# Performance work log

Measured on AMD Instinct MI355X. Metric: run time of the kernel, lower is better.

The kernel has to match this reference:

```python
import jax, jax.numpy as jnp
import numpy as np

B, T, D = 2, 2048, 2048
H, DH = 32, 64
GN_EPS = DH * 1e-5  # GroupNorm eps = head_dim * norm_eps


def _lora(x, A, Bm, bias, act):
    h = x @ A.T
    if act == 'tanh':
        h = jnp.tanh(h)
    elif act == 'sigmoid':
        h = jax.nn.sigmoid(h)
    y = h @ Bm.T
    if bias is not None:
        y = y + bias
    return y


def setup_inputs() -> dict:
    key = jax.random.key(0)
    ks = jax.random.split(key, 24)
    def nrm(i, shape, s):
        return jax.random.normal(ks[i], shape, jnp.float32) * s
    return {
        'hidden_states': nrm(0, (B, T, D), 1.0),
        'v_state': nrm(1, (B, T, D), 1.0),
        'x_x': nrm(2, (6, D), 0.3),
        'k_k': 0.85 + nrm(3, (D,), 0.05),
        'k_a': 1.0 + nrm(4, (D,), 0.05),
        'r_k': nrm(5, (H, DH), 0.1),
        'Wr': nrm(6, (D, D), 0.02),
        'Wk': nrm(7, (D, D), 0.02),
        'Wv': nrm(8, (D, D), 0.02),
        'Wo': nrm(9, (D, D), 0.02),
        'wA': nrm(10, (64, D), 0.02), 'wB': nrm(11, (D, 64), 0.02), 'wb': nrm(12, (D,), 0.5),
        'vA': nrm(13, (16, D), 0.02), 'vB': nrm(14, (D, 16), 0.02), 'vb': jnp.zeros((D,), jnp.float32),
        'aA': nrm(15, (64, D), 0.02), 'aB': nrm(16, (D, 64), 0.02), 'ab': jnp.zeros((D,), jnp.float32),
        'gA': nrm(17, (128, D), 0.02), 'gB': nrm(18, (D, 128), 0.02),
        'gn_w': jnp.ones((D,), jnp.float32), 'gn_b': jnp.zeros((D,), jnp.float32),
    }


def reference(hidden_states, v_state, x_x, k_k, k_a, r_k, Wr, Wk, Wv, Wo,
              wA, wB, wb, vA, vB, vb, aA, aB, ab, gA, gB, gn_w, gn_b):
    b, t, d = hidden_states.shape
    # time_shift: shifted[t] = x[t-1], shifted[0] = 0
    shifted = jnp.pad(hidden_states, ((0, 0), (1, 0), (0, 0)))[:, :t]
    delta = shifted - hidden_states
    xm = hidden_states[None] + delta[None] * x_x[:, None, None, :]  # [6,B,T,D]
    xr, xw, xk, xv, xa, xg = xm[0], xm[1], xm[2], xm[3], xm[4], xm[5]

    r = xr @ Wr.T
    w = -jax.nn.softplus(-_lora(xw, wA, wB, wb, 'tanh')) - 0.5  # log decay, < -0.5
    k = xk @ Wk.T
    v = xv @ Wv.T
    # layer_idx != 0: v = lerp(v, v_state, sigmoid(v_lora(xv)))
    v = v + jax.nn.sigmoid(_lora(xv, vA, vB, vb, None)) * (v_state - v)
    a = jax.nn.sigmoid(_lora(xa, aA, aB, ab, None))
    g = _lora(xg, gA, gB, None, 'sigmoid')

    kk = (k * k_k).reshape(b, t, H, DH)
    kk = kk / jnp.maximum(jnp.linalg.norm(kk, axis=-1, keepdims=True), 1e-12)
    k = k * (1.0 + (a - 1.0) * k_a)

    r_h = r.reshape(b, t, H, DH)
    w_h = w.reshape(b, t, H, DH)
    k_h = k.reshape(b, t, H, DH)
    v_h = v.reshape(b, t, H, DH)
    a_h = a.reshape(b, t, H, DH)
    tm = lambda x: jnp.swapaxes(x, 0, 1)  # [B,T,H,DH] -> [T,B,H,DH]

    # RWKV7 DPLR delta rule: S = diag(exp(w)) S; S += b (a^T S) + k v^T; o = r^T S
    def step(S, xs):
        q_t, w_t, k_t, v_t, at, bt = xs  # each [B,H,DH]
        S = S * jnp.exp(w_t)[..., None]
        sa = jnp.einsum('bhk,bhkv->bhv', at, S)
        S = S + bt[..., None] * sa[..., None, :] + k_t[..., None] * v_t[..., None, :]
        return S, jnp.einsum('bhk,bhkv->bhv', q_t, S)

    S0 = jnp.zeros((b, H, DH, DH), hidden_states.dtype)
    _, o = jax.lax.scan(step, S0,
                        (tm(r_h), tm(w_h), tm(k_h), tm(v_h), tm(-kk), tm(kk * a_h)))
    o = jnp.swapaxes(o, 0, 1)  # [B,T,H,DH]

    # GroupNorm over each head's channels
    mu = o.mean(-1, keepdims=True)
    var = jnp.mean((o - mu) ** 2, axis=-1, keepdims=True)
    on = ((o - mu) / jnp.sqrt(var + GN_EPS)).reshape(b, t, d) * gn_w + gn_b

    on = on + ((r_h * k_h * r_k).sum(-1, keepdims=True) * v_h).reshape(b, t, d)
    return (on * g) @ Wo.T
```

## Files before the change

kernel.cpp:

```cpp
#include <hip/hip_runtime.h>
#include <hip/hip_bf16.h>
#include <math.h>


typedef __attribute__((ext_vector_type(8))) unsigned short ushort8;
typedef __attribute__((ext_vector_type(8))) _Float16 f16x8;
typedef __attribute__((ext_vector_type(4))) float f32x4;
typedef __attribute__((ext_vector_type(2))) float f32x2;

__device__ inline unsigned short f2h(float f) {
    _Float16 h = (_Float16)f;
    return __builtin_bit_cast(unsigned short, h);
}
__device__ inline float h2f(unsigned short u) {
    return (float)__builtin_bit_cast(_Float16, u);
}
__device__ inline float sigm(float x) { return 1.f / (1.f + expf(-x)); }

template <int CTRL>
__device__ __forceinline__ float rrot(float x) {
    int xi = __builtin_bit_cast(int, x);
    int yi = __builtin_amdgcn_update_dpp(xi, xi, CTRL, 0xf, 0xf, true);
    return x + __builtin_bit_cast(float, yi);
}
// ... 19 lines not shown
    x = rrot<0x128>(x);
    return red32(red16(x));
}

__device__ __forceinline__ void gld16(void* lds, const void* g)
{
    __builtin_amdgcn_global_load_lds(
        (const __attribute__((address_space(1))) void*)g,
        (__attribute__((address_space(3))) void*)lds, 16, 0, 0);
}
__device__ __forceinline__ void gld4(void* lds, const void* g)
{
    __builtin_amdgcn_global_load_lds(
        (const __attribute__((address_space(1))) void*)g,
        (__attribute__((address_space(3))) void*)lds, 4, 0, 0);
}

__global__ void mixcvt6_h(const float* __restrict__ in, const float* __restrict__ x_x,
                          unsigned short* __restrict__ oR, unsigned short* __restrict__ oK,
                          unsigned short* __restrict__ ow, unsigned short* __restrict__ oa,
                          unsigned short* __restrict__ og, unsigned short* __restrict__ ov,
                          int T, int D, int total8)
{
    int i = blockIdx.x * 256 + threadIdx.x;
    if (i >= total8) return;
    const size_t e = (size_t)i * 8;
    float a[8];
    *(float4*)&a[0] = *(const float4*)(in + e);
    *(float4*)&a[4] = *(const float4*)(in + e + 4);
    const int m = (int)(e / D);
// ... 17 lines not shown
        rr[j] = f2h(a[j] + dl * xxr[j]);
        rk[j] = f2h(a[j] + dl * xxk[j]);
        rw[j] = f2h(a[j] + dl * xxw[j]);
        ra[j] = f2h(a[j] + dl * xxa[j]);
        rg[j] = f2h(a[j] + dl * xxg[j]);
        rv[j] = f2h(a[j] + dl * xxv[j]);
    }
    *(ushort8*)(oR + e) = rr;
    *(ushort8*)(oK + e) = rk;
    *(ushort8*)(ow + e) = rw;
    *(ushort8*)(oa + e) = ra;
    *(ushort8*)(og + e) = rg;
    *(ushort8*)(ov + e) = rv;
}

__global__ void wcvt2_h(const float* __restrict__ in0, const float* __restrict__ in1,
                        unsigned short* __restrict__ hi0, unsigned short* __restrict__ hi1,
                        int total8)
{
    int i = blockIdx.x * 256 + threadIdx.x;
    if (i >= total8) return;
    const float* in = (blockIdx.y == 0) ? in0 : in1;
    unsigned short* hi = (blockIdx.y == 0) ? hi0 : hi1;
    const size_t e = (size_t)i * 8;
    float a[8];
    *(float4*)&a[0] = *(const float4*)(in + e);
    *(float4*)&a[4] = *(const float4*)(in + e + 4);
    ushort8 h8;
    #pragma unroll
    for (int j = 0; j < 8; ++j) h8[j] = f2h(a[j]);
    *(ushort8*)(hi + e) = h8;
}

__global__ void wcvt_all(const float* __restrict__ Wr, const float* __restrict__ Wk,
                         const float* __restrict__ Wv, const float* __restrict__ wB,
                         const float* __restrict__ aB, const float* __restrict__ gB,
                         unsigned short* __restrict__ oWr, unsigned short* __restrict__ oWk,
                         unsigned short* __restrict__ oWv, unsigned short* __restrict__ owB,
                         unsigned short* __restrict__ oaB, unsigned short* __restrict__ ogB,
                         int nBig, int nSm, int nG)
{
    const int y = blockIdx.y;
    const float* in;
    unsigned short* hi;
    int lim;
    if (y == 0)      { in = Wr; hi = oWr; lim = nBig; }
    else if (y == 1) { in = Wk; hi = oWk; lim = nBig; }
    else if (y == 2) { in = Wv; hi = oWv; lim = nBig; }
    else if (y == 3) { in = wB; hi = owB; lim = nSm; }
    else if (y == 4) { in = aB; hi = oaB; lim = nSm; }
    else             { in = gB; hi = ogB; lim = nG; }
    int i = blockIdx.x * 256 + threadIdx.x;
    if (i >= lim) return;
    const size_t e = (size_t)i * 8;
    float a[8];
    *(float4*)&a[0] = *(const float4*)(in + e);
    *(float4*)&a[4] = *(const float4*)(in + e + 4);
    ushort8 h8;
    #pragma unroll
    for (int j = 0; j < 8; ++j) h8[j] = f2h(a[j]);
    *(ushort8*)(hi + e) = h8;
}

__global__ void wcvt_lora(const float* __restrict__ wA, const float* __restrict__ vA,
                          const float* __restrict__ aA, const float* __restrict__ gA,
                          unsigned short* __restrict__ WL, int K)
{
    const int z = blockIdx.y;
    int i = blockIdx.x * 256 + threadIdx.x;
    const size_t e = (size_t)i * 8;
    const int row = (int)(e / K);
    const int col = (int)(e % K);
    const int nv = (z == 0) ? 64 : (z == 1) ? 16 : (z == 2) ? 64 : 128;
    const float* src = (z == 0) ? wA : (z == 1) ? vA : (z == 2) ? aA : gA;
    ushort8 h8;
    if (row < nv) {
        float a[8];
        *(float4*)&a[0] = *(const float4*)(src + (size_t)row * K + col);
        *(float4*)&a[4] = *(const float4*)(src + (size_t)row * K + col + 4);
        #pragma unroll
        for (int j = 0; j < 8; ++j) h8[j] = f2h(a[j]);
    } else {
        #pragma unroll
        for (int j = 0; j < 8; ++j) h8[j] = 0;
    }
    *(ushort8*)(WL + (size_t)z * 128 * K + e) = h8;
}

#define GBM 128
#define GBN 128

template <int TERMS>
__global__ __launch_bounds__(256) void gemm_h2(
    const unsigned short* __restrict__ Ag,
    const unsigned short* __restrict__ Bhg, const unsigned short* __restrict__ Blg,
    float* __restrict__ C, int M, int N, int K, int mode,
    const float* __restrict__ HVp, const float* __restrict__ vBp,
    const float* __restrict__ bias, const float* __restrict__ aux,
    size_t sA, size_t sB, size_t sC)
{
    __shared__ unsigned short As[GBM * 32];
    __shared__ unsigned short Bhs[GBN * 32], Bls[GBN * 32];
    const int z = blockIdx.z;
    Ag  += (size_t)z * sA;
    Bhg += (size_t)z * sB;
    Blg += (size_t)z * sB;
    C   += (size_t)z * sC;
    const int tid = threadIdx.x;
    const int m0 = blockIdx.x * GBM;
    const int n0 = blockIdx.y * GBN;
    const int wave = tid >> 6, lane = tid & 63;
    const int wr = (wave >> 1) * 64, wc = (wave & 1) * 64;
    const int fr = lane & 15, fq = lane >> 4;

    f32x4 acc[4][4];
    #pragma unroll
    for (int i = 0; i < 4; ++i)
        #pragma unroll
        for (int j = 0; j < 4; ++j)
            acc[i][j] = (f32x4){0.f, 0.f, 0.f, 0.f};

    const unsigned short* gsrc;
    unsigned short* lbuf;
    int rofs, nld;
    if (wave == 0)      { gsrc = Ag;  lbuf = As;           rofs = m0;      nld = 4; }
    else if (wave == 1) { gsrc = Ag;  lbuf = As + 64 * 32; rofs = m0 + 64; nld = 4; }
    else if (wave == 2) { gsrc = Bhg; lbuf = Bhs;          rofs = n0;      nld = 8; }
    else                { gsrc = Blg; lbuf = Bls;          rofs = n0;      nld = (TERMS == 2) ? 8 : 0; }
    const unsigned short* gbase = gsrc + (size_t)(rofs + (lane >> 2)) * K + ((lane & 3) << 3);

    for (int k0 = 0; k0 < K; k0 += 32) {
        #pragma unroll
        for (int j = 0; j < 8; ++j)
            if (j < nld)
                gld16(lbuf + j * 16 * 32, gbase + (size_t)(j * 16) * K + k0);
        __syncthreads();

        f16x8 fa[4], fbh[4], fbl[4];
        #pragma unroll
        for (int m = 0; m < 4; ++m)
            fa[m] = *(const f16x8*)&As[(wr + m * 16 + fr) * 32 + fq * 8];
        #pragma unroll
        for (int n = 0; n < 4; ++n) {
            fbh[n] = *(const f16x8*)&Bhs[(wc + n * 16 + fr) * 32 + fq * 8];
            if constexpr (TERMS == 2)
                fbl[n] = *(const f16x8*)&Bls[(wc + n * 16 + fr) * 32 + fq * 8];
        }
        #pragma unroll
        for (int m = 0; m < 4; ++m)
            #pragma unroll
            for (int n = 0; n < 4; ++n) {
                acc[m][n] = __builtin_amdgcn_mfma_f32_16x16x32_f16(fa[m], fbh[n], acc[m][n], 0, 0, 0);
                if constexpr (TERMS == 2)
                    acc[m][n] = __builtin_amdgcn_mfma_f32_16x16x32_f16(fa[m], fbl[n], acc[m][n], 0, 0, 0);
            }
        __syncthreads();
    }

    #pragma unroll
    for (int m = 0; m < 4; ++m) {
        const int row = m0 + wr + m * 16 + fq * 4;
        #pragma unroll
        for (int n = 0; n < 4; ++n) {
            const int col = n0 + wc + n * 16 + fr;
            #pragma unroll
            for (int j = 0; j < 4; ++j) {
                const size_t idx = (size_t)(row + j) * N + col;
                float v = acc[m][n][j];
                if (mode == 4) {
                    const float* hv = HVp + (size_t)(row + j) * 16;
                    const float* vv = vBp + (size_t)col * 16;
                    float yv = 0.f;
                    #pragma unroll
                    for (int kk = 0; kk < 16; ++kk) yv = fmaf(hv[kk], vv[kk], yv);
                    const float sg = sigm(yv + bias[col]);
                    v = v + sg * (aux[idx] - v);
                } else if (mode == 3 && z == 0) {
                    v = 0.6065306597126334f * sigm(v + bias[col]);
                }
                C[idx] = v;
            }
        }
    }
}

__global__ __launch_bounds__(256) void gemm_rkv(
    const unsigned short* __restrict__ Xrk,
    const unsigned short* __restrict__ Xv,
    const unsigned short* __restrict__ Wr16, const unsigned short* __restrict__ Wk16,
    const unsigned short* __restrict__ Wv16,
    float* __restrict__ Cr, float* __restrict__ Ck, float* __restrict__ Cv,
    const float* __restrict__ HVp, const float* __restrict__ vBp,
    const float* __restrict__ vb, const float* __restrict__ vst,
    int M, int N, int K)
{
    __shared__ unsigned short As[GBM * 32];
    __shared__ unsigned short Bhs[GBN * 32];
    const int z = blockIdx.z;
    const unsigned short* Ag = (z == 0) ? Xrk : (z == 1) ? (Xrk + (size_t)M * K) : Xv;
    const unsigned short* Bg = (z == 0) ? Wr16 : (z == 1) ? Wk16 : Wv16;
    float* C = (z == 0) ? Cr : (z == 1) ? Ck : Cv;
    const int tid = threadIdx.x;
    const int m0 = blockIdx.x * GBM;
    const int n0 = blockIdx.y * GBN;
    const int wave = tid >> 6, lane = tid & 63;
    const int wr = (wave >> 1) * 64, wc = (wave & 1) * 64;
    const int fr = lane & 15, fq = lane >> 4;

    f32x4 acc[4][4];
    #pragma unroll
    for (int i = 0; i < 4; ++i)
        #pragma unroll
        for (int j = 0; j < 4; ++j)
            acc[i][j] = (f32x4){0.f, 0.f, 0.f, 0.f};

    const unsigned short* gsrc;
    unsigned short* lbuf;
    int rofs, nld;
    if (wave == 0)      { gsrc = Ag; lbuf = As;           rofs = m0;      nld = 4; }
    else if (wave == 1) { gsrc = Ag; lbuf = As + 64 * 32; rofs = m0 + 64; nld = 4; }
    else if (wave == 2) { gsrc = Bg; lbuf = Bhs;          rofs = n0;      nld = 8; }
    else                { gsrc = Bg; lbuf = Bhs;          rofs = n0;      nld = 0; }
    const unsigned short* gbase = gsrc + (size_t)(rofs + (lane >> 2)) * K + ((lane & 3) << 3);

    for (int k0 = 0; k0 < K; k0 += 32) {
        #pragma unroll
        for (int j = 0; j < 8; ++j)
            if (j < nld)
                gld16(lbuf + j * 16 * 32, gbase + (size_t)(j * 16) * K + k0);
        __syncthreads();

        f16x8 fa[4], fb[4];
        #pragma unroll
        for (int m = 0; m < 4; ++m)
            fa[m] = *(const f16x8*)&As[(wr + m * 16 + fr) * 32 + fq * 8];
        #pragma unroll
        for (int n = 0; n < 4; ++n)
            fb[n] = *(const f16x8*)&Bhs[(wc + n * 16 + fr) * 32 + fq * 8];
        #pragma unroll
        for (int m = 0; m < 4; ++m)
            #pragma unroll
            for (int n = 0; n < 4; ++n)
                acc[m][n] = __builtin_amdgcn_mfma_f32_16x16x32_f16(fa[m], fb[n], acc[m][n], 0, 0, 0);
        __syncthreads();
    }

    #pragma unroll
    for (int m = 0; m < 4; ++m) {
        const int row = m0 + wr + m * 16 + fq * 4;
        #pragma unroll
        for (int n = 0; n < 4; ++n) {
            const int col = n0 + wc + n * 16 + fr;
            #pragma unroll
            for (int j = 0; j < 4; ++j) {
                const size_t idx = (size_t)(row + j) * N + col;
                float v = acc[m][n][j];
                if (z == 2) {
                    const float* hv = HVp + (size_t)(row + j) * 16;
                    const float* vv = vBp + (size_t)col * 16;
                    float yv = 0.f;
                    #pragma unroll
                    for (int kk = 0; kk < 16; ++kk) yv = fmaf(hv[kk], vv[kk], yv);
                    const float sg = sigm(yv + vb[col]);
                    v = v + sg * (vst[idx] - v);
                }
                C[idx] = v;
            }
        }
    }
}

__global__ __launch_bounds__(256) void lora1_h(
    const unsigned short* __restrict__ Xbase,
    const unsigned short* __restrict__ WL,
    unsigned short* __restrict__ HW16, float* __restrict__ HV,
    unsigned short* __restrict__ HA16, unsigned short* __restrict__ HG16,
    int M, int K, size_t NE)
{
    __shared__ unsigned short As[GBM * 32];
    __shared__ unsigned short Bhs[GBN * 32];
    const int z = blockIdx.z;
    const size_t zofs = (z == 0) ? 0 : (z == 1) ? 3 * NE : (z == 2) ? NE : 2 * NE;
    const unsigned short* Ag = Xbase + zofs;
    const unsigned short* Bg = WL + (size_t)z * 128 * K;
    const int tid = threadIdx.x;
    const int m0 = blockIdx.x * GBM;
    const int wave = tid >> 6, lane = tid & 63;
    const int wr = (wave >> 1) * 64, wc = (wave & 1) * 64;
    const int fr = lane & 15, fq = lane >> 4;

    f32x4 acc[4][4];
    #pragma unroll
    for (int i = 0; i < 4; ++i)
        #pragma unroll
        for (int j = 0; j < 4; ++j)
            acc[i][j] = (f32x4){0.f, 0.f, 0.f, 0.f};

    const unsigned short* gsrc;
    unsigned short* lbuf;
    int rofs, nld;
    if (wave == 0)      { gsrc = Ag; lbuf = As;           rofs = m0;      nld = 4; }
    else if (wave == 1) { gsrc = Ag; lbuf = As + 64 * 32; rofs = m0 + 64; nld = 4; }
    else if (wave == 2) { gsrc = Bg; lbuf = Bhs;          rofs = 0;       nld = 8; }
    else                { gsrc = Bg; lbuf = Bhs;          rofs = 0;       nld = 0; }
    const unsigned short* gbase = gsrc + (size_t)(rofs + (lane >> 2)) * K + ((lane & 3) << 3);

    for (int k0 = 0; k0 < K; k0 += 32) {
        #pragma unroll
        for (int j = 0; j < 8; ++j)
            if (j < nld)
                gld16(lbuf + j * 16 * 32, gbase + (size_t)(j * 16) * K + k0);
        __syncthreads();

        f16x8 fa[4], fb[4];
        #pragma unroll
        for (int m = 0; m < 4; ++m)
            fa[m] = *(const f16x8*)&As[(wr + m * 16 + fr) * 32 + fq * 8];
        #pragma unroll
        for (int n = 0; n < 4; ++n)
            fb[n] = *(const f16x8*)&Bhs[(wc + n * 16 + fr) * 32 + fq * 8];
        #pragma unroll
        for (int m = 0; m < 4; ++m)
            #pragma unroll
            for (int n = 0; n < 4; ++n)
                acc[m][n] = __builtin_amdgcn_mfma_f32_16x16x32_f16(fa[m], fb[n], acc[m][n], 0, 0, 0);
        __syncthreads();
    }

    #pragma unroll
    for (int m = 0; m < 4; ++m) {
        const int row = m0 + wr + m * 16 + fq * 4;
        #pragma unroll
        for (int n = 0; n < 4; ++n) {
            const int col = wc + n * 16 + fr;
            #pragma unroll
            for (int j = 0; j < 4; ++j) {
                const float v = acc[m][n][j];
                const int r = row + j;
                if (z == 0)      { if (col < 64) HW16[(size_t)r * 64 + col] = f2h(tanhf(v)); }
                else if (z == 1) { if (col < 16) HV[(size_t)r * 16 + col] = v; }
                else if (z == 2) { if (col < 64) HA16[(size_t)r * 64 + col] = f2h(v); }
                else             { HG16[(size_t)r * 128 + col] = f2h(sigm(v)); }
// ... 169 lines not shown

    if (bid < 512) {
        if (tid >= 64) return;
        scan_core(smemf, bid, tid, EW, R, Kf, Vf, KK, BV, O, T, H);
        return;
    }
    if (bid < 1024) {
        unsigned short* As  = (unsigned short*)smemf;
        unsigned short* Bhs = As + GBM * 32;
        const int bid2 = bid - 512;
        const int m0 = (bid2 >> 4) * GBM;
        const int n0 = (bid2 & 15) * GBN;
        const int wave = tid >> 6, lane = tid & 63;
        const int wr = (wave >> 1) * 64, wc = (wave & 1) * 64;
        const int fr = lane & 15, fq = lane >> 4;
        const int K = 128;

        f32x4 acc[4][4];
        #pragma unroll
        for (int i = 0; i < 4; ++i)
            #pragma unroll
            for (int j = 0; j < 4; ++j)
                acc[i][j] = (f32x4){0.f, 0.f, 0.f, 0.f};

        const unsigned short* gsrc;
        unsigned short* lbuf;
        int rofs, nld;
        if (wave == 0)      { gsrc = HG16; lbuf = As;           rofs = m0;      nld = 4; }
        else if (wave == 1) { gsrc = HG16; lbuf = As + 64 * 32; rofs = m0 + 64; nld = 4; }
        else if (wave == 2) { gsrc = gb16; lbuf = Bhs;          rofs = n0;      nld = 8; }
        else                { gsrc = gb16; lbuf = Bhs;          rofs = n0;      nld = 0; }
        const unsigned short* gbase = gsrc + (size_t)(rofs + (lane >> 2)) * K + ((lane & 3) << 3);

        for (int k0 = 0; k0 < K; k0 += 32) {
            #pragma unroll
            for (int j = 0; j < 8; ++j)
                if (j < nld)
                    gld16(lbuf + j * 16 * 32, gbase + (size_t)(j * 16) * K + k0);
            __syncthreads();
            f16x8 fa[4], fb[4];
            #pragma unroll
            for (int m = 0; m < 4; ++m)
                fa[m] = *(const f16x8*)&As[(wr + m * 16 + fr) * 32 + fq * 8];
            #pragma unroll
            for (int n = 0; n < 4; ++n)
                fb[n] = *(const f16x8*)&Bhs[(wc + n * 16 + fr) * 32 + fq * 8];
            #pragma unroll
            for (int m = 0; m < 4; ++m)
                #pragma unroll
                for (int n = 0; n < 4; ++n)
                    acc[m][n] = __builtin_amdgcn_mfma_f32_16x16x32_f16(fa[m], fb[n], acc[m][n], 0, 0, 0);
            __syncthreads();
        }
        #pragma unroll
        for (int m = 0; m < 4; ++m) {
            const int row = m0 + wr + m * 16 + fq * 4;
            #pragma unroll
            for (int n = 0; n < 4; ++n) {
                const int col = n0 + wc + n * 16 + fr;
                #pragma unroll
                for (int j = 0; j < 4; ++j)
                    G16[(size_t)(row + j) * D + col] = f2h(acc[m][n][j]);
            }
        }
        return;
    }
    {
        int i = (bid - 1024) * 256 + tid;
// ... 88 lines not shown
    unsigned short* HA16 = HW16 + (size_t)M * 64;
    unsigned short* HG16 = HA16 + (size_t)M * 64;
    float* HV = (float*)(HG16 + (size_t)M * 128);
    float* W6 = SMALL + (size_t)M * 272;

    dim3 blk(256);
    const int nMix = (int)(NE / 8);
    const int nW   = (int)(DD / 8);
    const int nSm  = (int)(D * 64 / 8);
    const int nG   = (int)(D * 128 / 8);
    const float* nf = nullptr;

    unsigned short* X2   = (unsigned short*)W1;
    unsigned short* X4   = (unsigned short*)W4;
    unsigned short* WRK  = (unsigned short*)W3;
    unsigned short* WL   = (unsigned short*)W0;

    hipLaunchKernelGGL(mixcvt6_h, dim3(nMix / 256), blk, 0, stream,
                       hid, x_x, X2, X2 + NE, X4, X4 + NE, X4 + 2 * NE, X4 + 3 * NE, T, D, nMix);

    hipLaunchKernelGGL(wcvt_lora, dim3(128, 4), blk, 0, stream, wA, vA, aA, gA, WL, D);

    if (fused) {
        unsigned short* W6s  = (unsigned short*)W6;
        unsigned short* G16p = W6s;
        unsigned short* WvWo = W6s + NE;
        unsigned short* gb16 = W6s + NE + DD;
        unsigned short* wB16 = gb16 + (size_t)D * 128;
        unsigned short* aB16 = wB16 + (size_t)D * 64;

        hipLaunchKernelGGL(wcvt_all, dim3(nW / 256, 6), blk, 0, stream,
                           Wr, Wk, Wv, wB, aB, gB,
                           WRK, WRK + DD, WvWo, wB16, aB16, gb16, nW, nSm, nG);

        hipLaunchKernelGGL(lora1_h, dim3(M / GBM, 1, 4), blk, 0, stream,
                           X4, WL, HW16, HV, HA16, HG16, M, D, NE);

        hipLaunchKernelGGL(gemm_rkv, dim3(M / GBM, D / GBN, 3), blk, 0, stream,
                           X2, X4 + 3 * NE, WRK, WRK + DD, WvWo,
                           W0, W2, W3, HV, vB, vb, vst, M, D, D);

        hipLaunchKernelGGL((gemm_h2<1>), dim3(M / GBM, D / GBN, 2), blk, 0, stream,
                           HW16, wB16, wB16, W1, M, D, 64, 3, nf, nf, wb, nf,
                           (size_t)M * 64, (size_t)D * 64, 4 * NE);

        const int totalW = M * H;
        hipLaunchKernelGGL(ka_epi, dim3(totalW / 4), blk, 0, stream, W2, W5, W4, k_k, k_a, ab, totalW, H);

        hipLaunchKernelGGL(scan_fused, dim3(512 + 512 + 2048), blk, 0, stream,
                           W1, W0, W2, W3, W4, W5, out,
                           HG16, gb16, G16p, Wo, WvWo, nW, T, H, M, D);

        unsigned short* ON16 = (unsigned short*)W1;
        hipLaunchKernelGGL(gn_bonus, dim3(totalW / 4), blk, 0, stream, out, W0, W2, W3, nf, G16p, r_k, gnw, gnb, ON16, totalW, H, 64.f * 1e-5f);

        hipLaunchKernelGGL((gemm_h2<1>), dim3(M / GBM, D / GBN, 1), blk, 0, stream,
                           ON16, WvWo, WvWo, out, M, D, D, 0, nf, nf, nf, nf, 0, 0, 0);
    } else {
        hipLaunchKernelGGL(wcvt2_h, dim3(nW / 256, 2), blk, 0, stream, Wr, Wk, WRK, WRK + DD, nW);
        hipLaunchKernelGGL(lora1_h, dim3(M / GBM, 1, 4), blk, 0, stream,
                           X4, WL, HW16, HV, HA16, HG16, M, D, NE);
        hipLaunchKernelGGL((gemm_h2<1>), dim3(M / GBM, D / GBN, 2), blk, 0, stream,
                           X2, WRK, WRK, W0, M, D, D, 0, nf, nf, nf, nf,
                           NE, DD, 2 * NE);
        unsigned short* WvH = (unsigned short*)W4;
        hipLaunchKernelGGL(wcvt2_h, dim3(nW / 256, 1), blk, 0, stream, Wv, Wv, WvH, WvH, nW);
        hipLaunchKernelGGL((gemm_h2<1>), dim3(M / GBM, D / GBN, 1), blk, 0, stream,
                           X4 + 3 * NE, WvH, WvH, W3, M, D, D, 4, HV, vB, vb, vst, 0, 0, 0);
        unsigned short* wB16 = (unsigned short*)W4;
        unsigned short* aB16 = wB16 + (size_t)D * 64;
        hipLaunchKernelGGL(wcvt2_h, dim3(nSm / 256, 2), blk, 0, stream, wB, aB, wB16, aB16, nSm);
        hipLaunchKernelGGL((gemm_h2<1>), dim3(M / GBM, D / GBN, 2), blk, 0, stream,
                           HW16, wB16, wB16, W1, M, D, 64, 3, nf, nf, wb, nf,
                           (size_t)M * 64, (size_t)D * 64, 4 * NE);
        const int totalW = M * H;
        hipLaunchKernelGGL(ka_epi, dim3(totalW / 4), blk, 0, stream, W2, W5, W4, k_k, k_a, ab, totalW, H);
// ... 14 lines not shown
```

Measured before the change: 829.7 us.

## Merge prep conversions and independent GEMM launches into fewer mega-kernels

```diff
diff --git a/kernel.cpp b/kernel.cpp
--- a/kernel.cpp
+++ b/kernel.cpp
@@ -57,6 +57,416 @@
     __builtin_amdgcn_global_load_lds(
         (const __attribute__((address_space(1))) void*)g,
         (__attribute__((address_space(3))) void*)lds, 4, 0, 0);
+}
+
+__device__ __forceinline__ void gemm128_loop(
+    const unsigned short* __restrict__ Ag, const unsigned short* __restrict__ Bg,
+    unsigned short* As, unsigned short* Bhs,
+    int m0, int n0, int K, int tid, f32x4 (&acc)[4][4])
+{
+    const int wave = tid >> 6, lane = tid & 63;
+    const int wr = (wave >> 1) * 64, wc = (wave & 1) * 64;
+    const int fr = lane & 15, fq = lane >> 4;
+
+    const unsigned short* gsrc;
+    unsigned short* lbuf;
+    int rofs, nld;
+    if (wave == 0)      { gsrc = Ag; lbuf = As;           rofs = m0;      nld = 4; }
+    else if (wave == 1) { gsrc = Ag; lbuf = As + 64 * 32; rofs = m0 + 64; nld = 4; }
+    else if (wave == 2) { gsrc = Bg; lbuf = Bhs;          rofs = n0;      nld = 8; }
+    else                { gsrc = Bg; lbuf = Bhs;          rofs = n0;      nld = 0; }
+    const unsigned short* gbase = gsrc + (size_t)(rofs + (lane >> 2)) * K + ((lane & 3) << 3);
+
+    for (int k0 = 0; k0 < K; k0 += 32) {
+        #pragma unroll
+        for (int j = 0; j < 8; ++j)
+            if (j < nld)
+                gld16(lbuf + j * 16 * 32, gbase + (size_t)(j * 16) * K + k0);
+        __syncthreads();
+
+        f16x8 fa[4], fb[4];
+        #pragma unroll
+        for (int m = 0; m < 4; ++m)
+            fa[m] = *(const f16x8*)&As[(wr + m * 16 + fr) * 32 + fq * 8];
+        #pragma unroll
+        for (int n = 0; n < 4; ++n)
+            fb[n] = *(const f16x8*)&Bhs[(wc + n * 16 + fr) * 32 + fq * 8];
+        #pragma unroll
+        for (int m = 0; m < 4; ++m)
+            #pragma unroll
+            for (int n = 0; n < 4; ++n)
+                acc[m][n] = __builtin_amdgcn_mfma_f32_16x16x32_f16(fa[m], fb[n], acc[m][n], 0, 0, 0);
+        __syncthreads();
+    }
+}
+
+#define GBM 128
+#define GBN 128
+
+__global__ __launch_bounds__(256) void mega_prep(
+    const float* __restrict__ in, const float* __restrict__ x_x,
+    unsigned short* __restrict__ oR, unsigned short* __restrict__ oK,
+    unsigned short* __restrict__ ow, unsigned short* __restrict__ oa,
+    unsigned short* __restrict__ og, unsigned short* __restrict__ ov,
+    const float* __restrict__ wA, const float* __restrict__ vA,
+    const float* __restrict__ aA, const float* __restrict__ gA,
+    unsigned short* __restrict__ WL,
+    const float* __restrict__ Wr, const float* __restrict__ Wk,
+    const float* __restrict__ Wv, const float* __restrict__ wB,
+    const float* __restrict__ aB, const float* __restrict__ gB,
+    unsigned short* __restrict__ oWr, unsigned short* __restrict__ oWk,
+    unsigned short* __restrict__ oWv, unsigned short* __restrict__ owB,
+    unsigned short* __restrict__ oaB, unsigned short* __restrict__ ogB,
+    int T, int D, int nMix, int nBig, int nSm, int nG)
+{
+    const int bid = blockIdx.x;
+    const int tid = threadIdx.x;
+
+    if (bid < 4096) {
+        int i = bid * 256 + tid;
+        if (i >= nMix) return;
+        const size_t e = (size_t)i * 8;
+        float a[8];
+        *(float4*)&a[0] = *(const float4*)(in + e);
+        *(float4*)&a[4] = *(const float4*)(in + e + 4);
+        const int m = (int)(e / D);
+        const int d = (int)(e % D);
+        const int t = m % T;
+        float p[8] = {0.f,0.f,0.f,0.f,0.f,0.f,0.f,0.f};
+        if (t > 0) {
+            *(float4*)&p[0] = *(const float4*)(in + e - D);
+            *(float4*)&p[4] = *(const float4*)(in + e - D + 4);
+        }
+        const float* xxr = x_x + 0 * (size_t)D + d;
+        const float* xxw = x_x + 1 * (size_t)D + d;
+        const float* xxk = x_x + 2 * (size_t)D + d;
+        const float* xxv = x_x + 3 * (size_t)D + d;
+        const float* xxa = x_x + 4 * (size_t)D + d;
+        const float* xxg = x_x + 5 * (size_t)D + d;
+        ushort8 rr, rk, rw, ra, rg, rv;
+        #pragma unroll
+        for (int j = 0; j < 8; ++j) {
+            const float dl = p[j] - a[j];
+            rr[j] = f2h(a[j] + dl * xxr[j]);
+            rk[j] = f2h(a[j] + dl * xxk[j]);
+            rw[j] = f2h(a[j] + dl * xxw[j]);
+            ra[j] = f2h(a[j] + dl * xxa[j]);
+            rg[j] = f2h(a[j] + dl * xxg[j]);
+            rv[j] = f2h(a[j] + dl * xxv[j]);
+        }
+        *(ushort8*)(oR + e) = rr;
+        *(ushort8*)(oK + e) = rk;
+        *(ushort8*)(ow + e) = rw;
+        *(ushort8*)(oa + e) = ra;
+        *(ushort8*)(og + e) = rg;
+        *(ushort8*)(ov + e) = rv;
+        return;
+    }
+    if (bid < 4608) {
+        const int b2 = bid - 4096;
+        const int z = b2 >> 7;
+        int i = (b2 & 127) * 256 + tid;
+        const size_t e = (size_t)i * 8;
+        const int row = (int)(e / D);
+        const int col = (int)(e % D);
+        const int nv = (z == 0) ? 64 : (z == 1) ? 16 : (z == 2) ? 64 : 128;
+        const float* src = (z == 0) ? wA : (z == 1) ? vA : (z == 2) ? aA : gA;
+        ushort8 h8;
+        if (row < nv) {
+            float a[8];
+            *(float4*)&a[0] = *(const float4*)(src + (size_t)row * D + col);
+            *(float4*)&a[4] = *(const float4*)(src + (size_t)row * D + col + 4);
+            #pragma unroll
+            for (int j = 0; j < 8; ++j) h8[j] = f2h(a[j]);
+        } else {
+            #pragma unroll
+            for (int j = 0; j < 8; ++j) h8[j] = 0;
+        }
+        *(ushort8*)(WL + (size_t)z * 128 * D + e) = h8;
+        return;
+    }
+    int b2 = bid - 4608;
+    const float* win;
+    unsigned short* hi;
+    int i, lim;
+    if (b2 < 2048)                { win = Wr; hi = oWr; i = b2 * 256 + tid;         lim = nBig; }
+    else if ((b2 -= 2048) < 2048) { win = Wk; hi = oWk; i = b2 * 256 + tid;         lim = nBig; }
+    else if ((b2 -= 2048) < 2048) { win = Wv; hi = oWv; i = b2 * 256 + tid;         lim = nBig; }
+    else if ((b2 -= 2048) < 64)   { win = wB; hi = owB; i = b2 * 256 + tid;         lim = nSm; }
+    else if ((b2 -= 64) < 64)     { win = aB; hi = oaB; i = b2 * 256 + tid;         lim = nSm; }
+    else                          { win = gB; hi = ogB; i = (b2 - 64) * 256 + tid;  lim = nG; }
+    if (i >= lim) return;
+    const size_t e = (size_t)i * 8;
+    float a[8];
+    *(float4*)&a[0] = *(const float4*)(win + e);
+    *(float4*)&a[4] = *(const float4*)(win + e + 4);
+    ushort8 h8;
+    #pragma unroll
+    for (int j = 0; j < 8; ++j) h8[j] = f2h(a[j]);
+    *(ushort8*)(hi + e) = h8;
+}
+
+__global__ __launch_bounds__(256) void mega_b(
+    const unsigned short* __restrict__ Xrk,
+    const unsigned short* __restrict__ Wr16, const unsigned short* __restrict__ Wk16,
+    float* __restrict__ Cr, float* __restrict__ Ck,
+    const unsigned short* __restrict__ X4, const unsigned short* __restrict__ WL,
+    unsigned short* __restrict__ HW16, float* __restrict__ HV,
+    unsigned short* __restrict__ HA16, unsigned short* __restrict__ HG16,
+    int M, int D, size_t NE)
+{
+    __shared__ unsigned short As[GBM * 32];
+    __shared__ unsigned short Bhs[GBN * 32];
+    const int bid = blockIdx.x;
+    const int tid = threadIdx.x;
+    const int wave = tid >> 6, lane = tid & 63;
+    const int wr = (wave >> 1) * 64, wc = (wave & 1) * 64;
+    const int fr = lane & 15, fq = lane >> 4;
+
+    f32x4 acc[4][4];
+    #pragma unroll
+    for (int i = 0; i < 4; ++i)
+        #pragma unroll
+        for (int j = 0; j < 4; ++j)
+            acc[i][j] = (f32x4){0.f, 0.f, 0.f, 0.f};
+
+    if (bid < 1024) {
+        const int z = bid >> 9;
+        const int m0 = ((bid & 511) >> 4) * GBM;
+        const int n0 = (bid & 15) * GBN;
+        const unsigned short* Ag = Xrk + (size_t)z * NE;
+        const unsigned short* Bg = (z == 0) ? Wr16 : Wk16;
+        float* C = (z == 0) ? Cr : Ck;
+        gemm128_loop(Ag, Bg, As, Bhs, m0, n0, D, tid, acc);
+        #pragma unroll
+        for (int m = 0; m < 4; ++m) {
+            const int row = m0 + wr + m * 16 + fq * 4;
+            #pragma unroll
+            for (int n = 0; n < 4; ++n) {
+                const int col = n0 + wc + n * 16 + fr;
+                #pragma unroll
+                for (int j = 0; j < 4; ++j)
+                    C[(size_t)(row + j) * D + col] = acc[m][n][j];
+            }
+        }
+        return;
+    }
+    {
+        const int b2 = bid - 1024;
+        const int z = b2 >> 5;
+        const int m0 = (b2 & 31) * GBM;
+        const size_t zofs = (z == 0) ? 0 : (z == 1) ? 3 * NE : (z == 2) ? NE : 2 * NE;
+        const unsigned short* Ag = X4 + zofs;
+        const unsigned short* Bg = WL + (size_t)z * 128 * D;
+        gemm128_loop(Ag, Bg, As, Bhs, m0, 0, D, tid, acc);
+        #pragma unroll
+        for (int m = 0; m < 4; ++m) {
+            const int row = m0 + wr + m * 16 + fq * 4;
+            #pragma unroll
+            for (int n = 0; n < 4; ++n) {
+                const int col = wc + n * 16 + fr;
+                #pragma unroll
+                for (int j = 0; j < 4; ++j) {
+                    const float v = acc[m][n][j];
+                    const int r = row + j;
+                    if (z == 0)      { if (col < 64) HW16[(size_t)r * 64 + col] = f2h(tanhf(v)); }
+                    else if (z == 1) { if (col < 16) HV[(size_t)r * 16 + col] = v; }
+                    else if (z == 2) { if (col < 64) HA16[(size_t)r * 64 + col] = f2h(v); }
+                    else             { HG16[(size_t)r * 128 + col] = f2h(sigm(v)); }
+                }
+            }
+        }
+    }
+}
+
+__global__ __launch_bounds__(256) void mega_c(
+    const unsigned short* __restrict__ Xv, const unsigned short* __restrict__ Wv16,
+    float* __restrict__ Cv,
+    const float* __restrict__ HVp, const float* __restrict__ vBp,
+    const float* __restrict__ vb, const float* __restrict__ vst,
+    const unsigned short* __restrict__ HWA16,
+    const unsigned short* __restrict__ waB16,
+    float* __restrict__ EW, float* __restrict__ YA,
+    const float* __restrict__ wb,
+    int M, int D)
+{
+    __shared__ unsigned short As[GBM * 32];
+    __shared__ unsigned short Bhs[GBN * 32];
+    const int bid = blockIdx.x;
+    const int tid = threadIdx.x;
+    const int wave = tid >> 6, lane = tid & 63;
+    const int wr = (wave >> 1) * 64, wc = (wave & 1) * 64;
+    const int fr = lane & 15, fq = lane >> 4;
+
+    f32x4 acc[4][4];
+    #pragma unroll
+    for (int i = 0; i < 4; ++i)
+        #pragma unroll
+        for (int j = 0; j < 4; ++j)
+            acc[i][j] = (f32x4){0.f, 0.f, 0.f, 0.f};
+
+    if (bid < 512) {
+        const int m0 = (bid >> 4) * GBM;
+        const int n0 = (bid & 15) * GBN;
+        gemm128_loop(Xv, Wv16, As, Bhs, m0, n0, D, tid, acc);
+        #pragma unroll
+        for (int m = 0; m < 4; ++m) {
+            const int row = m0 + wr + m * 16 + fq * 4;
+            #pragma unroll
+            for (int n = 0; n < 4; ++n) {
+                const int col = n0 + wc + n * 16 + fr;
+                #pragma unroll
+                for (int j = 0; j < 4; ++j) {
+                    const size_t idx = (size_t)(row + j) * D + col;
+                    float v = acc[m][n][j];
+                    const float* hv = HVp + (size_t)(row + j) * 16;
+                    const float* vv = vBp + (size_t)col * 16;
+                    float yv = 0.f;
+                    #pragma unroll
+                    for (int kk = 0; kk < 16; ++kk) yv = fmaf(hv[kk], vv[kk], yv);
+                    const float sg = sigm(yv + vb[col]);
+                    Cv[idx] = v + sg * (vst[idx] - v);
+                }
+            }
+        }
+        return;
+    }
+    {
+        const int b2 = bid - 512;
+        const int z = b2 >> 9;
+        const int m0 = ((b2 & 511) >> 4) * GBM;
+        const int n0 = (b2 & 15) * GBN;
+        const unsigned short* Ag = HWA16 + (size_t)z * M * 64;
+        const unsigned short* Bg = waB16 + (size_t)z * D * 64;
+        float* C = (z == 0) ? EW : YA;
+        gemm128_loop(Ag, Bg, As, Bhs, m0, n0, 64, tid, acc);
+        #pragma unroll
+        for (int m = 0; m < 4; ++m) {
+            const int row = m0 + wr + m * 16 + fq * 4;
+            #pragma unroll
+            for (int n = 0; n < 4; ++n) {
+                const int col = n0 + wc + n * 16 + fr;
+                #pragma unroll
+                for (int j = 0; j < 4; ++j) {
+                    float v = acc[m][n][j];
+                    if (z == 0) v = 0.6065306597126334f * sigm(v + wb[col]);
+                    C[(size_t)(row + j) * D + col] = v;
+                }
+            }
+        }
+    }
+}
+
+template <int TERMS>
+__global__ __launch_bounds__(256) void gemm_h2(
+    const unsigned short* __restrict__ Ag,
+    const unsigned short* __restrict__ Bhg, const unsigned short* __restrict__ Blg,
+    float* __restrict__ C, int M, int N, int K, int mode,
+    const float* __restrict__ HVp, const float* __restrict__ vBp,
+    const float* __restrict__ bias, const float* __restrict__ aux,
+    size_t sA, size_t sB, size_t sC)
+{
+    __shared__ unsigned short As[GBM * 32];
+    __shared__ unsigned short Bhs[GBN * 32], Bls[GBN * 32];
+    const int z = blockIdx.z;
+    Ag  += (size_t)z * sA;
+    Bhg += (size_t)z * sB;
+    Blg += (size_t)z * sB;
+    C   += (size_t)z * sC;
+    const int tid = threadIdx.x;
+    const int m0 = blockIdx.x * GBM;
+    const int n0 = blockIdx.y * GBN;
+    const int wave = tid >> 6, lane = tid & 63;
+    const int wr = (wave >> 1) * 64, wc = (wave & 1) * 64;
+    const int fr = lane & 15, fq = lane >> 4;
+
+    f32x4 acc[4][4];
+    #pragma unroll
+    for (int i = 0; i < 4; ++i)
+        #pragma unroll
+        for (int j = 0; j < 4; ++j)
+            acc[i][j] = (f32x4){0.f, 0.f, 0.f, 0.f};
+
+    const unsigned short* gsrc;
+    unsigned short* lbuf;
+    int rofs, nld;
+    if (wave == 0)      { gsrc = Ag;  lbuf = As;           rofs = m0;      nld = 4; }
+    else if (wave == 1) { gsrc = Ag;  lbuf = As + 64 * 32; rofs = m0 + 64; nld = 4; }
+    else if (wave == 2) { gsrc = Bhg; lbuf = Bhs;          rofs = n0;      nld = 8; }
+    else                { gsrc = Blg; lbuf = Bls;          rofs = n0;      nld = (TERMS == 2) ? 8 : 0; }
+    const unsigned short* gbase = gsrc + (size_t)(rofs + (lane >> 2)) * K + ((lane & 3) << 3);
+
+    for (int k0 = 0; k0 < K; k0 += 32) {
+        #pragma unroll
+        for (int j = 0; j < 8; ++j)
+            if (j < nld)
+                gld16(lbuf + j * 16 * 32, gbase + (size_t)(j * 16) * K + k0);
+        __syncthreads();
+
+        f16x8 fa[4], fbh[4], fbl[4];
+        #pragma unroll
+        for (int m = 0; m < 4; ++m)
+            fa[m] = *(const f16x8*)&As[(wr + m * 16 + fr) * 32 + fq * 8];
+        #pragma unroll
+        for (int n = 0; n < 4; ++n) {
+            fbh[n] = *(const f16x8*)&Bhs[(wc + n * 16 + fr) * 32 + fq * 8];
+            if constexpr (TERMS == 2)
+                fbl[n] = *(const f16x8*)&Bls[(wc + n * 16 + fr) * 32 + fq * 8];
+        }
+        #pragma unroll
+        for (int m = 0; m < 4; ++m)
+            #pragma unroll
+            for (int n = 0; n < 4; ++n) {
+                acc[m][n] = __builtin_amdgcn_mfma_f32_16x16x32_f16(fa[m], fbh[n], acc[m][n], 0, 0, 0);
+                if constexpr (TERMS == 2)
+                    acc[m][n] = __builtin_amdgcn_mfma_f32_16x16x32_f16(fa[m], fbl[n], acc[m][n], 0, 0, 0);
+            }
+        __syncthreads();
+    }
+
+    #pragma unroll
+    for (int m = 0; m < 4; ++m) {
+        const int row = m0 + wr + m * 16 + fq * 4;
+        #pragma unroll
+        for (int n = 0; n < 4; ++n) {
+            const int col = n0 + wc + n * 16 + fr;
+            #pragma unroll
+            for (int j = 0; j < 4; ++j) {
+                const size_t idx = (size_t)(row + j) * N + col;
+                float v = acc[m][n][j];
+                if (mode == 4) {
+                    const float* hv = HVp + (size_t)(row + j) * 16;
+                    const float* vv = vBp + (size_t)col * 16;
+                    float yv = 0.f;
+                    #pragma unroll
+                    for (int kk = 0; kk < 16; ++kk) yv = fmaf(hv[kk], vv[kk], yv);
+                    const float sg = sigm(yv + bias[col]);
+                    v = v + sg * (aux[idx] - v);
+                } else if (mode == 3 && z == 0) {
+                    v = 0.6065306597126334f * sigm(v + bias[col]);
+                }
+                C[idx] = v;
+            }
+        }
+    }
+}
+
+__global__ void wcvt2_h(const float* __restrict__ in0, const float* __restrict__ in1,
+                        unsigned short* __restrict__ hi0, unsigned short* __restrict__ hi1,
+                        int total8)
+{
+    int i = blockIdx.x * 256 + threadIdx.x;
+    if (i >= total8) return;
+    const float* in = (blockIdx.y == 0) ? in0 : in1;
+    unsigned short* hi = (blockIdx.y == 0) ? hi0 : hi1;
+    const size_t e = (size_t)i * 8;
+    float a[8];
+    *(float4*)&a[0] = *(const float4*)(in + e);
+    *(float4*)&a[4] = *(const float4*)(in + e + 4);
+    ushort8 h8;
+    #pragma unroll
+    for (int j = 0; j < 8; ++j) h8[j] = f2h(a[j]);
+    *(ushort8*)(hi + e) = h8;
 }
 
 __global__ void mixcvt6_h(const float* __restrict__ in, const float* __restrict__ x_x,
@@ -104,54 +514,6 @@
     *(ushort8*)(ov + e) = rv;
 }
 
-__global__ void wcvt2_h(const float* __restrict__ in0, const float* __restrict__ in1,
-                        unsigned short* __restrict__ hi0, unsigned short* __restrict__ hi1,
-                        int total8)
-{
-    int i = blockIdx.x * 256 + threadIdx.x;
-    if (i >= total8) return;
-    const float* in = (blockIdx.y == 0) ? in0 : in1;
-    unsigned short* hi = (blockIdx.y == 0) ? hi0 : hi1;
-    const size_t e = (size_t)i * 8;
-    float a[8];
-    *(float4*)&a[0] = *(const float4*)(in + e);
-    *(float4*)&a[4] = *(const float4*)(in + e + 4);
-    ushort8 h8;
-    #pragma unroll
-    for (int j = 0; j < 8; ++j) h8[j] = f2h(a[j]);
-    *(ushort8*)(hi + e) = h8;
-}
-
-__global__ void wcvt_all(const float* __restrict__ Wr, const float* __restrict__ Wk,
-                         const float* __restrict__ Wv, const float* __restrict__ wB,
-                         const float* __restrict__ aB, const float* __restrict__ gB,
-                         unsigned short* __restrict__ oWr, unsigned short* __restrict__ oWk,
-                         unsigned short* __restrict__ oWv, unsigned short* __restrict__ owB,
-                         unsigned short* __restrict__ oaB, unsigned short* __restrict__ ogB,
-                         int nBig, int nSm, int nG)
-{
-    const int y = blockIdx.y;
-    const float* in;
-    unsigned short* hi;
-    int lim;
-    if (y == 0)      { in = Wr; hi = oWr; lim = nBig; }
-    else if (y == 1) { in = Wk; hi = oWk; lim = nBig; }
-    else if (y == 2) { in = Wv; hi = oWv; lim = nBig; }
-    else if (y == 3) { in = wB; hi = owB; lim = nSm; }
-    else if (y == 4) { in = aB; hi = oaB; lim = nSm; }
-    else             { in = gB; hi = ogB; lim = nG; }
-    int i = blockIdx.x * 256 + threadIdx.x;
-    if (i >= lim) return;
-    const size_t e = (size_t)i * 8;
-    float a[8];
-    *(float4*)&a[0] = *(const float4*)(in + e);
-    *(float4*)&a[4] = *(const float4*)(in + e + 4);
-    ushort8 h8;
-    #pragma unroll
-    for (int j = 0; j < 8; ++j) h8[j] = f2h(a[j]);
-    *(ushort8*)(hi + e) = h8;
-}
-
 __global__ void wcvt_lora(const float* __restrict__ wA, const float* __restrict__ vA,
                           const float* __restrict__ aA, const float* __restrict__ gA,
                           unsigned short* __restrict__ WL, int K)
@@ -177,189 +539,6 @@
     *(ushort8*)(WL + (size_t)z * 128 * K + e) = h8;
 }
 
-#define GBM 128
-#define GBN 128
-
-template <int TERMS>
-__global__ __launch_bounds__(256) void gemm_h2(
-    const unsigned short* __restrict__ Ag,
-    const unsigned short* __restrict__ Bhg, const unsigned short* __restrict__ Blg,
-    float* __restrict__ C, int M, int N, int K, int mode,
-    const float* __restrict__ HVp, const float* __restrict__ vBp,
-    const float* __restrict__ bias, const float* __restrict__ aux,
-    size_t sA, size_t sB, size_t sC)
-{
-    __shared__ unsigned short As[GBM * 32];
-    __shared__ unsigned short Bhs[GBN * 32], Bls[GBN * 32];
-    const int z = blockIdx.z;
-    Ag  += (size_t)z * sA;
-    Bhg += (size_t)z * sB;
-    Blg += (size_t)z * sB;
-    C   += (size_t)z * sC;
-    const int tid = threadIdx.x;
-    const int m0 = blockIdx.x * GBM;
-    const int n0 = blockIdx.y * GBN;
-    const int wave = tid >> 6, lane = tid & 63;
-    const int wr = (wave >> 1) * 64, wc = (wave & 1) * 64;
-    const int fr = lane & 15, fq = lane >> 4;
-
-    f32x4 acc[4][4];
-    #pragma unroll
-    for (int i = 0; i < 4; ++i)
-        #pragma unroll
-        for (int j = 0; j < 4; ++j)
-            acc[i][j] = (f32x4){0.f, 0.f, 0.f, 0.f};
-
-    const unsigned short* gsrc;
-    unsigned short* lbuf;
-    int rofs, nld;
-    if (wave == 0)      { gsrc = Ag;  lbuf = As;           rofs = m0;      nld = 4; }
-    else if (wave == 1) { gsrc = Ag;  lbuf = As + 64 * 32; rofs = m0 + 64; nld = 4; }
-    else if (wave == 2) { gsrc = Bhg; lbuf = Bhs;          rofs = n0;      nld = 8; }
-    else                { gsrc = Blg; lbuf = Bls;          rofs = n0;      nld = (TERMS == 2) ? 8 : 0; }
-    const unsigned short* gbase = gsrc + (size_t)(rofs + (lane >> 2)) * K + ((lane & 3) << 3);
-
-    for (int k0 = 0; k0 < K; k0 += 32) {
-        #pragma unroll
-        for (int j = 0; j < 8; ++j)
-            if (j < nld)
-                gld16(lbuf + j * 16 * 32, gbase + (size_t)(j * 16) * K + k0);
-        __syncthreads();
-
-        f16x8 fa[4], fbh[4], fbl[4];
-        #pragma unroll
-        for (int m = 0; m < 4; ++m)
-            fa[m] = *(const f16x8*)&As[(wr + m * 16 + fr) * 32 + fq * 8];
-        #pragma unroll
-        for (int n = 0; n < 4; ++n) {
-            fbh[n] = *(const f16x8*)&Bhs[(wc + n * 16 + fr) * 32 + fq * 8];
-            if constexpr (TERMS == 2)
-                fbl[n] = *(const f16x8*)&Bls[(wc + n * 16 + fr) * 32 + fq * 8];
-        }
-        #pragma unroll
-        for (int m = 0; m < 4; ++m)
-            #pragma unroll
-            for (int n = 0; n < 4; ++n) {
-                acc[m][n] = __builtin_amdgcn_mfma_f32_16x16x32_f16(fa[m], fbh[n], acc[m][n], 0, 0, 0);
-                if constexpr (TERMS == 2)
-                    acc[m][n] = __builtin_amdgcn_mfma_f32_16x16x32_f16(fa[m], fbl[n], acc[m][n], 0, 0, 0);
-            }
-        __syncthreads();
-    }
-
-    #pragma unroll
-    for (int m = 0; m < 4; ++m) {
-        const int row = m0 + wr + m * 16 + fq * 4;
-        #pragma unroll
-        for (int n = 0; n < 4; ++n) {
-            const int col = n0 + wc + n * 16 + fr;
-            #pragma unroll
-            for (int j = 0; j < 4; ++j) {
-                const size_t idx = (size_t)(row + j) * N + col;
-                float v = acc[m][n][j];
-                if (mode == 4) {
-                    const float* hv = HVp + (size_t)(row + j) * 16;
-                    const float* vv = vBp + (size_t)col * 16;
-                    float yv = 0.f;
-                    #pragma unroll
-                    for (int kk = 0; kk < 16; ++kk) yv = fmaf(hv[kk], vv[kk], yv);
-                    const float sg = sigm(yv + bias[col]);
-                    v = v + sg * (aux[idx] - v);
-                } else if (mode == 3 && z == 0) {
-                    v = 0.6065306597126334f * sigm(v + bias[col]);
-                }
-                C[idx] = v;
-            }
-        }
-    }
-}
-
-__global__ __launch_bounds__(256) void gemm_rkv(
-    const unsigned short* __restrict__ Xrk,
-    const unsigned short* __restrict__ Xv,
-    const unsigned short* __restrict__ Wr16, const unsigned short* __restrict__ Wk16,
-    const unsigned short* __restrict__ Wv16,
-    float* __restrict__ Cr, float* __restrict__ Ck, float* __restrict__ Cv,
-    const float* __restrict__ HVp, const float* __restrict__ vBp,
-    const float* __restrict__ vb, const float* __restrict__ vst,
-    int M, int N, int K)
-{
-    __shared__ unsigned short As[GBM * 32];
-    __shared__ unsigned short Bhs[GBN * 32];
-    const int z = blockIdx.z;
-    const unsigned short* Ag = (z == 0) ? Xrk : (z == 1) ? (Xrk + (size_t)M * K) : Xv;
-    const unsigned short* Bg = (z == 0) ? Wr16 : (z == 1) ? Wk16 : Wv16;
-    float* C = (z == 0) ? Cr : (z == 1) ? Ck : Cv;
-    const int tid = threadIdx.x;
-    const int m0 = blockIdx.x * GBM;
-    const int n0 = blockIdx.y * GBN;
-    const int wave = tid >> 6, lane = tid & 63;
-    const int wr = (wave >> 1) * 64, wc = (wave & 1) * 64;
-    const int fr = lane & 15, fq = lane >> 4;
-
-    f32x4 acc[4][4];
-    #pragma unroll
-    for (int i = 0; i < 4; ++i)
-        #pragma unroll
-        for (int j = 0; j < 4; ++j)
-            acc[i][j] = (f32x4){0.f, 0.f, 0.f, 0.f};
-
-    const unsigned short* gsrc;
-    unsigned short* lbuf;
-    int rofs, nld;
-    if (wave == 0)      { gsrc = Ag; lbuf = As;           rofs = m0;      nld = 4; }
-    else if (wave == 1) { gsrc = Ag; lbuf = As + 64 * 32; rofs = m0 + 64; nld = 4; }
-    else if (wave == 2) { gsrc = Bg; lbuf = Bhs;          rofs = n0;      nld = 8; }
-    else                { gsrc = Bg; lbuf = Bhs;          rofs = n0;      nld = 0; }
-    const unsigned short* gbase = gsrc + (size_t)(rofs + (lane >> 2)) * K + ((lane & 3) << 3);
-
-    for (int k0 = 0; k0 < K; k0 += 32) {
-        #pragma unroll
-        for (int j = 0; j < 8; ++j)
-            if (j < nld)
-                gld16(lbuf + j * 16 * 32, gbase + (size_t)(j * 16) * K + k0);
-        __syncthreads();
-
-        f16x8 fa[4], fb[4];
-        #pragma unroll
-        for (int m = 0; m < 4; ++m)
-            fa[m] = *(const f16x8*)&As[(wr + m * 16 + fr) * 32 + fq * 8];
-        #pragma unroll
-        for (int n = 0; n < 4; ++n)
-            fb[n] = *(const f16x8*)&Bhs[(wc + n * 16 + fr) * 32 + fq * 8];
-        #pragma unroll
-        for (int m = 0; m < 4; ++m)
-            #pragma unroll
-            for (int n = 0; n < 4; ++n)
-                acc[m][n] = __builtin_amdgcn_mfma_f32_16x16x32_f16(fa[m], fb[n], acc[m][n], 0, 0, 0);
-        __syncthreads();
-    }
-
-    #pragma unroll
-    for (int m = 0; m < 4; ++m) {
-        const int row = m0 + wr + m * 16 + fq * 4;
-        #pragma unroll
-        for (int n = 0; n < 4; ++n) {
-            const int col = n0 + wc + n * 16 + fr;
-            #pragma unroll
-            for (int j = 0; j < 4; ++j) {
-                const size_t idx = (size_t)(row + j) * N + col;
-                float v = acc[m][n][j];
-                if (z == 2) {
-                    const float* hv = HVp + (size_t)(row + j) * 16;
-                    const float* vv = vBp + (size_t)col * 16;
-                    float yv = 0.f;
-                    #pragma unroll
-                    for (int kk = 0; kk < 16; ++kk) yv = fmaf(hv[kk], vv[kk], yv);
-                    const float sg = sigm(yv + vb[col]);
-                    v = v + sg * (vst[idx] - v);
-                }
-                C[idx] = v;
-            }
-        }
-    }
-}
-
 __global__ __launch_bounds__(256) void lora1_h(
     const unsigned short* __restrict__ Xbase,
     const unsigned short* __restrict__ WL,
@@ -386,36 +565,7 @@
         for (int j = 0; j < 4; ++j)
             acc[i][j] = (f32x4){0.f, 0.f, 0.f, 0.f};
 
-    const unsigned short* gsrc;
-    unsigned short* lbuf;
-    int rofs, nld;
-    if (wave == 0)      { gsrc = Ag; lbuf = As;           rofs = m0;      nld = 4; }
-    else if (wave == 1) { gsrc = Ag; lbuf = As + 64 * 32; rofs = m0 + 64; nld = 4; }
-    else if (wave == 2) { gsrc = Bg; lbuf = Bhs;          rofs = 0;       nld = 8; }
-    else                { gsrc = Bg; lbuf = Bhs;          rofs = 0;       nld = 0; }
-    const unsigned short* gbase = gsrc + (size_t)(rofs + (lane >> 2)) * K + ((lane & 3) << 3);
-
-    for (int k0 = 0; k0 < K; k0 += 32) {
-        #pragma unroll
-        for (int j = 0; j < 8; ++j)
-            if (j < nld)
-                gld16(lbuf + j * 16 * 32, gbase + (size_t)(j * 16) * K + k0);
-        __syncthreads();
-
-        f16x8 fa[4], fb[4];
-        #pragma unroll
-        for (int m = 0; m < 4; ++m)
-            fa[m] = *(const f16x8*)&As[(wr + m * 16 + fr) * 32 + fq * 8];
-        #pragma unroll
-        for (int n = 0; n < 4; ++n)
-            fb[n] = *(const f16x8*)&Bhs[(wc + n * 16 + fr) * 32 + fq * 8];
-        #pragma unroll
-        for (int m = 0; m < 4; ++m)
-            #pragma unroll
-            for (int n = 0; n < 4; ++n)
-                acc[m][n] = __builtin_amdgcn_mfma_f32_16x16x32_f16(fa[m], fb[n], acc[m][n], 0, 0, 0);
-        __syncthreads();
-    }
+    gemm128_loop(Ag, Bg, As, Bhs, m0, 0, K, tid, acc);
 
     #pragma unroll
     for (int m = 0; m < 4; ++m) {
@@ -615,7 +765,6 @@
         const int wave = tid >> 6, lane = tid & 63;
         const int wr = (wave >> 1) * 64, wc = (wave & 1) * 64;
         const int fr = lane & 15, fq = lane >> 4;
-        const int K = 128;
 
         f32x4 acc[4][4];
         #pragma unroll
@@ -624,35 +773,8 @@
             for (int j = 0; j < 4; ++j)
                 acc[i][j] = (f32x4){0.f, 0.f, 0.f, 0.f};
 
-        const unsigned short* gsrc;
-        unsigned short* lbuf;
-        int rofs, nld;
-        if (wave == 0)      { gsrc = HG16; lbuf = As;           rofs = m0;      nld = 4; }
-        else if (wave == 1) { gsrc = HG16; lbuf = As + 64 * 32; rofs = m0 + 64; nld = 4; }
-        else if (wave == 2) { gsrc = gb16; lbuf = Bhs;          rofs = n0;      nld = 8; }
-        else                { gsrc = gb16; lbuf = Bhs;          rofs = n0;      nld = 0; }
-        const unsigned short* gbase = gsrc + (size_t)(rofs + (lane >> 2)) * K + ((lane & 3) << 3);
-
-        for (int k0 = 0; k0 < K; k0 += 32) {
-            #pragma unroll
-            for (int j = 0; j < 8; ++j)
-                if (j < nld)
-                    gld16(lbuf + j * 16 * 32, gbase + (size_t)(j * 16) * K + k0);
-            __syncthreads();
-            f16x8 fa[4], fb[4];
-            #pragma unroll
-            for (int m = 0; m < 4; ++m)
-                fa[m] = *(const f16x8*)&As[(wr + m * 16 + fr) * 32 + fq * 8];
-            #pragma unroll
-            for (int n = 0; n < 4; ++n)
-                fb[n] = *(const f16x8*)&Bhs[(wc + n * 16 + fr) * 32 + fq * 8];
-            #pragma unroll
-            for (int m = 0; m < 4; ++m)
-                #pragma unroll
-                for (int n = 0; n < 4; ++n)
-                    acc[m][n] = __builtin_amdgcn_mfma_f32_16x16x32_f16(fa[m], fb[n], acc[m][n], 0, 0, 0);
-            __syncthreads();
-        }
+        gemm128_loop(HG16, gb16, As, Bhs, m0, n0, 128, tid, acc);
+
         #pragma unroll
         for (int m = 0; m < 4; ++m) {
             const int row = m0 + wr + m * 16 + fq * 4;
@@ -771,12 +893,6 @@
     unsigned short* X2   = (unsigned short*)W1;
     unsigned short* X4   = (unsigned short*)W4;
     unsigned short* WRK  = (unsigned short*)W3;
-    unsigned short* WL   = (unsigned short*)W0;
-
-    hipLaunchKernelGGL(mixcvt6_h, dim3(nMix / 256), blk, 0, stream,
-                       hid, x_x, X2, X2 + NE, X4, X4 + NE, X4 + 2 * NE, X4 + 3 * NE, T, D, nMix);
-
-    hipLaunchKernelGGL(wcvt_lora, dim3(128, 4), blk, 0, stream, wA, vA, aA, gA, WL, D);
 
     if (fused) {
         unsigned short* W6s  = (unsigned short*)W6;
@@ -785,27 +901,28 @@
         unsigned short* gb16 = W6s + NE + DD;
         unsigned short* wB16 = gb16 + (size_t)D * 128;
         unsigned short* aB16 = wB16 + (size_t)D * 64;
-
-        hipLaunchKernelGGL(wcvt_all, dim3(nW / 256, 6), blk, 0, stream,
+        unsigned short* WL   = aB16 + (size_t)D * 64;
+
+        hipLaunchKernelGGL(mega_prep, dim3(4096 + 512 + 3 * 2048 + 64 + 64 + 128), blk, 0, stream,
+                           hid, x_x, X2, X2 + NE, X4, X4 + NE, X4 + 2 * NE, X4 + 3 * NE,
+                           wA, vA, aA, gA, WL,
                            Wr, Wk, Wv, wB, aB, gB,
-                           WRK, WRK + DD, WvWo, wB16, aB16, gb16, nW, nSm, nG);
-
-        hipLaunchKernelGGL(lora1_h, dim3(M / GBM, 1, 4), blk, 0, stream,
+                           WRK, WRK + DD, WvWo, wB16, aB16, gb16,
+                           T, D, nMix, nW, nSm, nG);
+
+        hipLaunchKernelGGL(mega_b, dim3(1024 + 128), blk, 0, stream,
+                           X2, WRK, WRK + DD, W0, W2,
                            X4, WL, HW16, HV, HA16, HG16, M, D, NE);
 
-        hipLaunchKernelGGL(gemm_rkv, dim3(M / GBM, D / GBN, 3), blk, 0, stream,
-                           X2, X4 + 3 * NE, WRK, WRK + DD, WvWo,
-                           W0, W2, W3, HV, vB, vb, vst, M, D, D);
-
-        hipLaunchKernelGGL((gemm_h2<1>), dim3(M / GBM, D / GBN, 2), blk, 0, stream,
-                           HW16, wB16, wB16, W1, M, D, 64, 3, nf, nf, wb, nf,
-                           (size_t)M * 64, (size_t)D * 64, 4 * NE);
+        hipLaunchKernelGGL(mega_c, dim3(512 + 1024), blk, 0, stream,
+                           X4 + 3 * NE, WvWo, W3, HV, vB, vb, vst,
+                           HW16, wB16, W1, W4, wb, M, D);
 
         const int totalW = M * H;
-        hipLaunchKernelGGL(ka_epi, dim3(totalW / 4), blk, 0, stream, W2, W5, W4, k_k, k_a, ab, totalW, H);
+        hipLaunchKernelGGL(ka_epi, dim3(totalW / 4), blk, 0, stream, W2, W4, W5, k_k, k_a, ab, totalW, H);
 
         hipLaunchKernelGGL(scan_fused, dim3(512 + 512 + 2048), blk, 0, stream,
-                           W1, W0, W2, W3, W4, W5, out,
+                           W1, W0, W2, W3, W5, W4, out,
                            HG16, gb16, G16p, Wo, WvWo, nW, T, H, M, D);
 
         unsigned short* ON16 = (unsigned short*)W1;
@@ -814,9 +931,13 @@
         hipLaunchKernelGGL((gemm_h2<1>), dim3(M / GBM, D / GBN, 1), blk, 0, stream,
                            ON16, WvWo, WvWo, out, M, D, D, 0, nf, nf, nf, nf, 0, 0, 0);
     } else {
+        unsigned short* WL0 = (unsigned short*)W0;
+        hipLaunchKernelGGL(mixcvt6_h, dim3(nMix / 256), blk, 0, stream,
+                           hid, x_x, X2, X2 + NE, X4, X4 + NE, X4 + 2 * NE, X4 + 3 * NE, T, D, nMix);
+        hipLaunchKernelGGL(wcvt_lora, dim3(128, 4), blk, 0, stream, wA, vA, aA, gA, WL0, D);
         hipLaunchKernelGGL(wcvt2_h, dim3(nW / 256, 2), blk, 0, stream, Wr, Wk, WRK, WRK + DD, nW);
         hipLaunchKernelGGL(lora1_h, dim3(M / GBM, 1, 4), blk, 0, stream,
-                           X4, WL, HW16, HV, HA16, HG16, M, D, NE);
+                           X4, WL0, HW16, HV, HA16, HG16, M, D, NE);
         hipLaunchKernelGGL((gemm_h2<1>), dim3(M / GBM, D / GBN, 2), blk, 0, stream,
                            X2, WRK, WRK, W0, M, D, D, 0, nf, nf, nf, nf,
                            NE, DD, 2 * NE);
```

Result: slower. 954.9 us (+15.1%).
